# Kernel tuning notes

Hardware: AMD Instinct MI355X
Metric: run time of the kernel (lower is better)

Reference implementation:

```python
import jax, jax.numpy as jnp
import numpy as np

N = 240000
B = 2
GRID = (480, 360, 32)
NUM_CLASS = 20
IGNORE_LABEL = 0
MINB = np.array([0.0, -np.pi, -4.0], np.float32)
MAXB = np.array([50.0, np.pi, 2.0], np.float32)
EPS = 1e-5


def setup_inputs() -> dict:
    key = jax.random.key(0)
    ks = jax.random.split(key, 32)
    d = {}
    d['pt_fea'] = jax.random.normal(ks[0], (N, 6), jnp.float32)
    # cylindrical coords (rho, phi, z) uniformly inside the volume
    u = jax.random.uniform(ks[1], (N, 3), jnp.float32)
    d['xyz'] = u * jnp.asarray(MAXB - MINB) + jnp.asarray(MINB)
    d['batch_idx'] = jnp.sort(jax.random.randint(ks[2], (N,), 0, B)).astype(jnp.int64)
    d['pt_lab'] = jax.random.randint(ks[3], (N,), 0, NUM_CLASS).astype(jnp.int64)
    d['shuffled_ind'] = jnp.arange(N, dtype=jnp.int64)  # identity perm (deterministic)
    i = 4
    for name, c in [('bn0', 9), ('bn1', 64), ('bn2', 128), ('bn3', 256)]:
        d[name + '_g'] = jax.random.uniform(ks[i], (c,), jnp.float32, 0.5, 1.5); i += 1
        d[name + '_b'] = jax.random.normal(ks[i], (c,), jnp.float32) * 0.1; i += 1
        d[name + '_m'] = jax.random.normal(ks[i], (c,), jnp.float32) * 0.1; i += 1
        d[name + '_v'] = jax.random.uniform(ks[i], (c,), jnp.float32, 0.5, 1.5); i += 1
    for name, (fi, fo) in [('1', (9, 64)), ('2', (64, 128)), ('3', (128, 256)), ('4', (256, 256))]:
        d['w' + name] = jax.random.normal(ks[i], (fi, fo), jnp.float32) / np.sqrt(fi); i += 1
        d['b' + name] = jax.random.normal(ks[i], (fo,), jnp.float32) * 0.01; i += 1
    d['wc'] = jax.random.normal(ks[i], (256, 16), jnp.float32) / 16.0; i += 1
    d['bc'] = jax.random.normal(ks[i], (16,), jnp.float32) * 0.01
    return d


def _bn(x, g, b, m, v):
    return (x - m) * (g * jax.lax.rsqrt(v + EPS)) + b


def _ppmodel(feat, bn0_g, bn0_b, bn0_m, bn0_v, w1, b1, bn1_g, bn1_b, bn1_m, bn1_v,
             w2, b2, bn2_g, bn2_b, bn2_m, bn2_v, w3, b3, bn3_g, bn3_b, bn3_m, bn3_v, w4, b4):
    x = _bn(feat, bn0_g, bn0_b, bn0_m, bn0_v)
    x = jax.nn.relu(_bn(x @ w1 + b1, bn1_g, bn1_b, bn1_m, bn1_v))
    x = jax.nn.relu(_bn(x @ w2 + b2, bn2_g, bn2_b, bn2_m, bn2_v))
    x = jax.nn.relu(_bn(x @ w3 + b3, bn3_g, bn3_b, bn3_m, bn3_v))
    return x @ w4 + b4  # [N, 256]


def reference(pt_fea, xyz, batch_idx, pt_lab, shuffled_ind,
              bn0_g, bn0_b, bn0_m, bn0_v, w1, b1, bn1_g, bn1_b, bn1_m, bn1_v,
              w2, b2, bn2_g, bn2_b, bn2_m, bn2_v, w3, b3, bn3_g, bn3_b, bn3_m, bn3_v,
              w4, b4, wc, bc):
    minb = jnp.asarray(MINB)
    maxb = jnp.asarray(MAXB)
    grid = jnp.asarray(np.array(GRID, np.float32))
    intervals = (maxb - minb) / (grid - 1.0)

    clamped = jnp.clip(xyz, minb, maxb)
    ind = jnp.floor((clamped - minb) / intervals).astype(jnp.int32)  # [N,3]
    voxel_centers = (ind.astype(jnp.float32) + 0.5) * intervals + minb
    rel_xyz = xyz - voxel_centers
    feat = jnp.concatenate([rel_xyz, pt_fea], axis=1)  # [N,9]

    bi = batch_idx.astype(jnp.int32)
    counts = jnp.full((B,) + GRID + (NUM_CLASS,), IGNORE_LABEL, jnp.int32)
    counts = counts.at[bi, ind[:, 0], ind[:, 1], ind[:, 2], pt_lab].add(1)
    voxel_labels = jnp.argmax(counts, axis=-1).astype(jnp.int32)  # [B,480,360,32]

    feat = feat[shuffled_ind]

    flat = ((bi.astype(jnp.int64) * GRID[0] + ind[:, 0]) * GRID[1] + ind[:, 1]) * GRID[2] + ind[:, 2]
    unq, unq_inv = jnp.unique(flat, size=N, fill_value=-1, return_inverse=True)
    unq_inv = unq_inv.reshape(-1)

    processed = _ppmodel(feat, bn0_g, bn0_b, bn0_m, bn0_v, w1, b1, bn1_g, bn1_b, bn1_m, bn1_v,
                         w2, b2, bn2_g, bn2_b, bn2_m, bn2_v, w3, b3, bn3_g, bn3_b, bn3_m, bn3_v, w4, b4)
    pooled = jax.ops.segment_max(processed, unq_inv, num_segments=N)
    seg_cnt = jax.ops.segment_sum(jnp.ones((N,), jnp.float32), unq_inv, num_segments=N)
    pooled = jnp.where(seg_cnt[:, None] > 0, pooled, 0.0)  # zero out empty (padded) segments

    processed_pooled = jax.nn.relu(pooled @ wc + bc)  # fea_compression

    cat_pt_ind = jnp.concatenate([batch_idx[:, None], ind.astype(jnp.int64)], axis=1)
    return (unq, processed_pooled, voxel_labels, cat_pt_ind)
```

## Files before the change

kernel.cpp:

```cpp
#include <hip/hip_runtime.h>
#include <stdint.h>

#define N_PTS 240000
#define NV    11059200
#define NWORDS 172800
#define NB_PT 938
#define NB_WORD 675
#define NBLK_MLP 3750
#define PA 264

typedef __bf16 bf16x8 __attribute__((ext_vector_type(8)));
typedef short  short8 __attribute__((ext_vector_type(8)));
typedef float  f32x4  __attribute__((ext_vector_type(4)));

__device__ __forceinline__ unsigned short f2bf(float f) {
  unsigned u = __builtin_bit_cast(unsigned, f);
  return (unsigned short)((u + 0x7FFFu + ((u >> 16) & 1u)) >> 16);
}
__device__ __forceinline__ float bf2f(unsigned short h) {
  unsigned u = ((unsigned)h) << 16;
  return __builtin_bit_cast(float, u);
}

__global__ void prep_vox_kernel(
    const float* __restrict__ bng0, const float* __restrict__ bnb0, const float* __restrict__ bnm0, const float* __restrict__ bnv0,
    const float* __restrict__ bng1, const float* __restrict__ bnb1, const float* __restrict__ bnm1, const float* __restrict__ bnv1,
    const float* __restrict__ bng2, const float* __restrict__ bnb2, const float* __restrict__ bnm2, const float* __restrict__ bnv2,
    const float* __restrict__ bng3, const float* __restrict__ bnb3, const float* __restrict__ bnm3, const float* __restrict__ bnv3,
    const float* __restrict__ w1, const float* __restrict__ b1,
    const float* __restrict__ w2, const float* __restrict__ b2,
    const float* __restrict__ w3, const float* __restrict__ b3,
    const float* __restrict__ w4, const float* __restrict__ wc,
    float* __restrict__ s0, float* __restrict__ t0, float* __restrict__ w1e, float* __restrict__ be1,
    float* __restrict__ be2, float* __restrict__ be3,
    unsigned short* __restrict__ w2t, unsigned short* __restrict__ w3t, unsigned short* __restrict__ w4t,
    unsigned short* __restrict__ wct,
    const float* __restrict__ xyz, const int* __restrict__ bidx,
    unsigned* __restrict__ flatkeys, unsigned long long* __restrict__ bitmap,
    float* __restrict__ out_cat, float* __restrict__ out_unq)
{
  if (blockIdx.x < 256) {
    const int id = blockIdx.x * 256 + threadIdx.x;
    { int c = id >> 8, k = id & 255; w4t[c * 256 + k] = f2bf(w4[k * 256 + c]); }
    if (id < 32768) { int c = id >> 7, k = id & 127;
      float s = bng3[c] * rsqrtf(bnv3[c] + 1e-5f);
      w3t[c * 128 + k] = f2bf(w3[k * 256 + c] * s); }
    if (id < 8192) { int c = id >> 6, k = id & 63;
      float s = bng2[c] * rsqrtf(bnv2[c] + 1e-5f);
      w2t[c * 64 + k] = f2bf(w2[k * 128 + c] * s); }
    if (id < 4096) { int c = id >> 8, k = id & 255;
      wct[c * 256 + k] = f2bf(wc[k * 16 + c]); }
    if (id < 576) { int k = id / 64, c = id % 64;
      float s = bng1[c] * rsqrtf(bnv1[c] + 1e-5f);
      w1e[k * 64 + c] = w1[k * 64 + c] * s; }
    if (id < 64)  { float s = bng1[id] * rsqrtf(bnv1[id] + 1e-5f); be1[id] = (b1[id] - bnm1[id]) * s + bnb1[id]; }
    if (id < 128) { float s = bng2[id] * rsqrtf(bnv2[id] + 1e-5f); be2[id] = (b2[id] - bnm2[id]) * s + bnb2[id]; }
    if (id < 256) { float s = bng3[id] * rsqrtf(bnv3[id] + 1e-5f); be3[id] = (b3[id] - bnm3[id]) * s + bnb3[id]; }
    if (id < 9)   { float s = bng0[id] * rsqrtf(bnv0[id] + 1e-5f); s0[id] = s; t0[id] = bnb0[id] - bnm0[id] * s; }
    return;
  }
  const int j = (blockIdx.x - 256) * 256 + threadIdx.x;
  if (j >= N_PTS) return;
  out_unq[j] = -1.0f;
  const float PI_F = 3.14159265358979323846f;
  const float minb[3] = {0.0f, -PI_F, -4.0f};
  const float maxb[3] = {50.0f, PI_F, 2.0f};
  const float gm1[3]  = {479.0f, 359.0f, 31.0f};
  int ind[3];
  #pragma unroll
  for (int d = 0; d < 3; ++d) {
    float itv = (maxb[d] - minb[d]) / gm1[d];
    float x  = xyz[(size_t)j * 3 + d];
    float cl = fminf(fmaxf(x, minb[d]), maxb[d]);
    ind[d] = (int)floorf((cl - minb[d]) / itv);
  }
  const int bi = bidx[j];
  const unsigned flat = ((unsigned)(bi * 480 + ind[0]) * 360u + (unsigned)ind[1]) * 32u + (unsigned)ind[2];
  flatkeys[j] = flat;
  atomicOr(&bitmap[flat >> 6], 1ull << (flat & 63u));
  float* oc = out_cat + (size_t)j * 4;
  oc[0] = (float)bi; oc[1] = (float)ind[0]; oc[2] = (float)ind[1]; oc[3] = (float)ind[2];
}

__global__ void reduce_words(const unsigned long long* __restrict__ bm, unsigned* __restrict__ bsums) {
  __shared__ unsigned sh[256];
  const int w = blockIdx.x * 256 + threadIdx.x;
  sh[threadIdx.x] = (unsigned)__popcll(bm[w]);
  __syncthreads();
  for (int s = 128; s > 0; s >>= 1) { if (threadIdx.x < s) sh[threadIdx.x] += sh[threadIdx.x + s]; __syncthreads(); }
  if (threadIdx.x == 0) bsums[blockIdx.x] = sh[0];
}

__global__ void scan_small(unsigned* __restrict__ d, int n) {
  __shared__ unsigned sh[1024];
  const int t = threadIdx.x;
  unsigned own = (t < n) ? d[t] : 0u;
  sh[t] = own; __syncthreads();
  for (int off = 1; off < 1024; off <<= 1) {
    unsigned v = (t >= off) ? sh[t - off] : 0u;
    __syncthreads(); sh[t] += v; __syncthreads();
  }
  if (t < n) d[t] = sh[t] - own;
}

__global__ void scatter_unq(const unsigned long long* __restrict__ bm, const unsigned* __restrict__ bsums,
                            unsigned* __restrict__ wordpref, unsigned* __restrict__ unqvals,
                            float* __restrict__ out_unq) {
  __shared__ unsigned sh[256];
  const int t = threadIdx.x;
  const int w = blockIdx.x * 256 + t;
  unsigned long long word = bm[w];
  unsigned own = (unsigned)__popcll(word);
  sh[t] = own; __syncthreads();
  for (int off = 1; off < 256; off <<= 1) {
    unsigned v = (t >= off) ? sh[t - off] : 0u;
    __syncthreads(); sh[t] += v; __syncthreads();
  }
  unsigned r = bsums[blockIdx.x] + sh[t] - own;
  wordpref[w] = r;
  while (word) {
    int b = __builtin_ctzll(word);
    unsigned id = (unsigned)w * 64u + (unsigned)b;
    unqvals[r] = id;
    out_unq[r] = (float)id;
    ++r;
    word &= word - 1;
  }
}

__global__ void inv_kernel(const unsigned* __restrict__ flatkeys, const unsigned long long* __restrict__ bm,
                           const unsigned* __restrict__ wordpref, const int* __restrict__ ptlab,
                           unsigned* __restrict__ unq_inv, unsigned* __restrict__ cnt, unsigned* __restrict__ counts) {
  const int j = blockIdx.x * 256 + threadIdx.x;
  if (j >= N_PTS) return;
  const unsigned f = flatkeys[j];
  const unsigned w = f >> 6, b = f & 63u;
  const unsigned r = wordpref[w] + (unsigned)__popcll(bm[w] & ((1ull << b) - 1ull));
  unq_inv[j] = r;
  atomicAdd(&cnt[r], 1u);
  const unsigned lab = (unsigned)ptlab[j];
  atomicAdd(&counts[(size_t)r * 10 + (lab >> 1)], 1u << ((lab & 1u) * 16));
}

__global__ void reduce_cnt(const unsigned* __restrict__ cnt, unsigned* __restrict__ bsums) {
  __shared__ unsigned sh[256];
  const int j = blockIdx.x * 256 + threadIdx.x;
  sh[threadIdx.x] = (j < N_PTS) ? cnt[j] : 0u;
  __syncthreads();
  for (int s = 128; s > 0; s >>= 1) { if (threadIdx.x < s) sh[threadIdx.x] += sh[threadIdx.x + s]; __syncthreads(); }
  if (threadIdx.x == 0) bsums[blockIdx.x] = sh[0];
}
__global__ void scan_cnt(const unsigned* __restrict__ cnt, const unsigned* __restrict__ bsums,
                         unsigned* __restrict__ off, unsigned* __restrict__ cur) {
  __shared__ unsigned sh[256];
  const int t = threadIdx.x;
  const int j = blockIdx.x * 256 + t;
  unsigned own = (j < N_PTS) ? cnt[j] : 0u;
  sh[t] = own; __syncthreads();
  for (int o = 1; o < 256; o <<= 1) {
    unsigned v = (t >= o) ? sh[t - o] : 0u;
    __syncthreads(); sh[t] += v; __syncthreads();
  }
  if (j < N_PTS) { unsigned e = bsums[blockIdx.x] + sh[t] - own; off[j] = e; cur[j] = e; }
}

__global__ void plist_labels_kernel(const unsigned* __restrict__ unq_inv, unsigned* __restrict__ cur,
                                    unsigned* __restrict__ plist,
                                    const unsigned* __restrict__ cnt, const unsigned* __restrict__ counts,
                                    const unsigned* __restrict__ unqvals, const float* __restrict__ bc,
                                    float* __restrict__ out_lab, float* __restrict__ out_pooled) {
  const int j = blockIdx.x * 256 + threadIdx.x;
  if (j >= N_PTS) return;
  plist[atomicAdd(&cur[unq_inv[j]], 1u)] = (unsigned)j;
  const int u = j;
  if (cnt[u] == 0) {
    #pragma unroll
    for (int c = 0; c < 16; ++c) out_pooled[(size_t)u * 16 + c] = fmaxf(bc[c], 0.f);
    return;
  }
  const unsigned* c = counts + (size_t)u * 10;
  int best = 0; unsigned bv = c[0] & 0xFFFFu;
  #pragma unroll
  for (int l = 1; l < 20; ++l) {
    unsigned v = (c[l >> 1] >> ((l & 1) * 16)) & 0xFFFFu;
    if (v > bv) { bv = v; best = l; }
  }
  out_lab[unqvals[u]] = (float)best;
}

template<int K, int C, bool RELU, bool MIDB>
__device__ __forceinline__ void gemm_stage(
    const unsigned short* __restrict__ Wt,
    const float* __restrict__ bias,
    const unsigned short* in,
    unsigned short* outp,
    int wave, int l15, int quad)
{
  constexpr int KC = K / 32;
  constexpr int NT = C / 64;
  f32x4 acc[4][NT];
  #pragma unroll
  for (int mt = 0; mt < 4; ++mt)
    #pragma unroll
    for (int nt = 0; nt < NT; ++nt) acc[mt][nt] = (f32x4){0.f, 0.f, 0.f, 0.f};
  const unsigned short* wp[NT];
  #pragma unroll
  for (int nt = 0; nt < NT; ++nt)
    wp[nt] = Wt + (size_t)(wave * 16 * NT + nt * 16 + l15) * K + quad * 8;
  #pragma unroll
  for (int kc = 0; kc < KC; ++kc) {
    bf16x8 b[NT];
    #pragma unroll
    for (int nt = 0; nt < NT; ++nt)
      b[nt] = __builtin_bit_cast(bf16x8, *(const short8*)(wp[nt] + kc * 32));
    #pragma unroll
    for (int mt = 0; mt < 4; ++mt) {
      bf16x8 a = __builtin_bit_cast(bf16x8, *(const short8*)&in[(mt * 16 + l15) * PA + kc * 32 + quad * 8]);
      #pragma unroll
      for (int nt = 0; nt < NT; ++nt)
        acc[mt][nt] = __builtin_amdgcn_mfma_f32_16x16x32_bf16(b[nt], a, acc[mt][nt], 0, 0, 0);
    }
  }
  if (MIDB) __syncthreads();
  #pragma unroll
  for (int mt = 0; mt < 4; ++mt)
    #pragma unroll
    for (int nt = 0; nt < NT; ++nt) {
      const int cbase = wave * 16 * NT + nt * 16 + quad * 4;
      const f32x4 bs = *(const f32x4*)&bias[cbase];
      unsigned short h[4];
      #pragma unroll
      for (int r = 0; r < 4; ++r) {
        float y = acc[mt][nt][r] + bs[r];
        if (RELU) y = fmaxf(y, 0.f);
        h[r] = f2bf(y);
      }
      uint2 pk; pk.x = (unsigned)h[0] | ((unsigned)h[1] << 16);
      pk.y = (unsigned)h[2] | ((unsigned)h[3] << 16);
      *(uint2*)&outp[(mt * 16 + l15) * PA + cbase] = pk;
    }
  __syncthreads();
}

__global__ __launch_bounds__(256, 4) void mlp_pool_kernel(
    const float* __restrict__ ptfea, const float* __restrict__ xyz, const int* __restrict__ shuf,
    const unsigned* __restrict__ plist, const unsigned* __restrict__ unq_inv,
    const unsigned* __restrict__ offv, const unsigned* __restrict__ cnt,
    const float* __restrict__ s0, const float* __restrict__ t0,
    const float* __restrict__ w1e, const float* __restrict__ be1,
    const unsigned short* __restrict__ w2t, const float* __restrict__ be2,
    const unsigned short* __restrict__ w3t, const float* __restrict__ be3,
    const unsigned short* __restrict__ w4t, const float* __restrict__ b4,
    const unsigned short* __restrict__ wct, const float* __restrict__ bc,
    unsigned short* __restrict__ partials, float* __restrict__ out_pooled)
{
  __shared__ __align__(16) unsigned short buf[64 * PA];
  __shared__ int segs[64];
  __shared__ int jrows[64];
  __shared__ int s_alast;
  __shared__ int s_nrun;
  __shared__ unsigned short s_runs[32];
  __shared__ unsigned char s_lead[64], s_comp[64];
  const int tid  = threadIdx.x;
  const int wave = tid >> 6, lane = tid & 63;
  const int l15 = lane & 15, quad = lane >> 4;
  const int row0 = blockIdx.x * 64;

  if (tid == 0) { s_alast = 0; s_nrun = 0; }
  if (lane < 16) {
    const int r = wave * 16 + lane;
    int j = (int)plist[row0 + r];
    jrows[r] = j;
    segs[r] = (int)unq_inv[j];
  }

  {
    const int r = wave * 16 + (lane >> 2), part = lane & 3;
    const int sj = shuf[jrows[r]];
    const float PI_F = 3.14159265358979323846f;
    const float minb[3] = {0.0f, -PI_F, -4.0f};
    const float maxb[3] = {50.0f, PI_F, 2.0f};
    const float gm1[3]  = {479.0f, 359.0f, 31.0f};
    float x0[9];
    #pragma unroll
    for (int d = 0; d < 3; ++d) {
      float itv = (maxb[d] - minb[d]) / gm1[d];
      float x   = xyz[(size_t)sj * 3 + d];
      float cl  = fminf(fmaxf(x, minb[d]), maxb[d]);
      float fi  = floorf((cl - minb[d]) / itv);
      float center = (fi + 0.5f) * itv + minb[d];
      x0[d] = (x - center) * s0[d] + t0[d];
    }
    #pragma unroll
    for (int d = 0; d < 6; ++d) x0[3 + d] = ptfea[(size_t)sj * 6 + d] * s0[3 + d] + t0[3 + d];
    unsigned short h[16];
    #pragma unroll
    for (int ci = 0; ci < 16; ++ci) {
      float acc = be1[part * 16 + ci];
      #pragma unroll
      for (int k = 0; k < 9; ++k) acc += x0[k] * w1e[k * 64 + part * 16 + ci];
      h[ci] = f2bf(fmaxf(acc, 0.0f));
    }
    *(short8*)&buf[r * PA + part * 16]     = *(short8*)&h[0];
    *(short8*)&buf[r * PA + part * 16 + 8] = *(short8*)&h[8];
  }
  __syncthreads();

  gemm_stage< 64, 128, true,  false>(w2t, be2, buf,       buf + 136, wave, l15, quad);
  gemm_stage<128, 256, true,  true >(w3t, be3, buf + 136, buf,       wave, l15, quad);
  gemm_stage<256, 256, false, true >(w4t, b4,  buf,       buf,       wave, l15, quad);

  if (tid < 64) {
    const int r = tid;
    bool lead = (r == 0) || (segs[r] != segs[r - 1]);
    s_lead[r] = lead ? 1 : 0;
    unsigned char comp = 0;
    int e = r + 1;
    if (lead) {
      atomicMax(&s_alast, r);
      while (e < 64 && segs[e] == segs[r]) ++e;
      const unsigned s = (unsigned)segs[r];
      comp = (offv[s] == (unsigned)(row0 + r) && offv[s] + cnt[s] == (unsigned)(row0 + e)) ? 1 : 0;
    }
    s_comp[r] = comp;
    const bool multi = lead && (e - r) > 1;
    unsigned long long mm = __ballot(multi);
    if (multi) {
      int idx = (int)__popcll(mm & ((1ull << r) - 1ull));
      s_runs[idx] = (unsigned short)((r << 8) | e);
    }
    if (tid == 0) s_nrun = (int)__popcll(mm);
  }
  __syncthreads();

  {
    const int n = s_nrun;
    for (int i = 0; i < n; ++i) {
      const int re = s_runs[i];
      const int r = re >> 8, e = re & 255;
      float m = bf2f(buf[r * PA + tid]);
      for (int rr = r + 1; rr < e; ++rr) m = fmaxf(m, bf2f(buf[rr * PA + tid]));
      buf[r * PA + tid] = f2bf(m);
    }
  }
  __syncthreads();

  {
    const int c = tid;
    const int alast = s_alast;
    const size_t b2 = (size_t)blockIdx.x * 2;
    if (!s_comp[0])     partials[b2 * 256 + c]       = buf[0 * PA + c];
    if (!s_comp[alast]) partials[(b2 + 1) * 256 + c] = buf[alast * PA + c];
  }

  {
    const unsigned short* wp = wct + l15 * 256 + quad * 8;
    f32x4 acc = (f32x4){0.f, 0.f, 0.f, 0.f};
    #pragma unroll
    for (int kc = 0; kc < 256; kc += 32) {
      bf16x8 w = __builtin_bit_cast(bf16x8, *(const short8*)(wp + kc));
      bf16x8 x = __builtin_bit_cast(bf16x8, *(const short8*)&buf[(wave * 16 + l15) * PA + kc + quad * 8]);
      acc = __builtin_amdgcn_mfma_f32_16x16x32_bf16(w, x, acc, 0, 0, 0);
    }
    const int r1 = wave * 16 + l15;
    if (s_lead[r1] && s_comp[r1]) {
      const f32x4 bcv = *(const f32x4*)&bc[quad * 4];
      f32x4 v;
      #pragma unroll
      for (int r = 0; r < 4; ++r) v[r] = fmaxf(acc[r] + bcv[r], 0.f);
      *(f32x4*)&out_pooled[(size_t)segs[r1] * 16 + quad * 4] = v;
    }
  }
}

__global__ __launch_bounds__(256) void merge_kernel(
    const unsigned* __restrict__ plist, const unsigned* __restrict__ unq_inv,
    const unsigned* __restrict__ offv, const unsigned* __restrict__ cnt,
    const unsigned short* __restrict__ partials,
    const float* __restrict__ wc, const float* __restrict__ bc,
    float* __restrict__ out_pooled)
{
  __shared__ float pooled[256];
  __shared__ float psum[256];
  const int b = blockIdx.x;
  const unsigned s = unq_inv[plist[(size_t)b * 64 + 63]];
  const unsigned o = offv[s], e = o + cnt[s];
  if ((o >> 6) != (unsigned)b) return;
  if (e <= (unsigned)(b + 1) * 64) return;
  const int B1 = (int)((e - 1) >> 6);
  const int c = threadIdx.x;
  float m = bf2f(partials[((size_t)2 * b + 1) * 256 + c]);
  for (int bb = b + 1; bb <= B1; ++bb)
    m = fmaxf(m, bf2f(partials[(size_t)2 * bb * 256 + c]));
  pooled[c] = m;
  __syncthreads();
  const int co = c & 15, kg = c >> 4;
  float p = 0.f;
  #pragma unroll
  for (int k = kg * 16; k < kg * 16 + 16; ++k) p += pooled[k] * wc[k * 16 + co];
  psum[c] = p;
  __syncthreads();
  if (c < 16) {
    float acc = bc[c];
    #pragma unroll
    for (int g = 0; g < 16; ++g) acc += psum[g * 16 + c];
    out_pooled[(size_t)s * 16 + c] = fmaxf(acc, 0.f);
  }
}

extern "C" void kernel_launch(void* const* d_in, const int* in_sizes, int n_in,
                              void* d_out, int out_size, void* d_ws, size_t ws_size,
                              hipStream_t stream)
{
  const float* pt_fea = (const float*)d_in[0];
  const float* xyz    = (const float*)d_in[1];
  const int*   bidx   = (const int*)d_in[2];
  const int*   ptlab  = (const int*)d_in[3];
  const int*   shuf   = (const int*)d_in[4];
  const float* bng0 = (const float*)d_in[5],  *bnb0 = (const float*)d_in[6],  *bnm0 = (const float*)d_in[7],  *bnv0 = (const float*)d_in[8];
  const float* bng1 = (const float*)d_in[9],  *bnb1 = (const float*)d_in[10], *bnm1 = (const float*)d_in[11], *bnv1 = (const float*)d_in[12];
  const float* bng2 = (const float*)d_in[13], *bnb2 = (const float*)d_in[14], *bnm2 = (const float*)d_in[15], *bnv2 = (const float*)d_in[16];
  const float* bng3 = (const float*)d_in[17], *bnb3 = (const float*)d_in[18], *bnm3 = (const float*)d_in[19], *bnv3 = (const float*)d_in[20];
  const float* w1 = (const float*)d_in[21], *b1 = (const float*)d_in[22];
  const float* w2 = (const float*)d_in[23], *b2 = (const float*)d_in[24];
  const float* w3 = (const float*)d_in[25], *b3 = (const float*)d_in[26];
  const float* w4 = (const float*)d_in[27], *b4 = (const float*)d_in[28];
  const float* wc = (const float*)d_in[29], *bc = (const float*)d_in[30];

  float* out        = (float*)d_out;
  float* out_unq    = out;
  float* out_pooled = out + 240000;
  float* out_lab    = out + 4080000;
  float* out_cat    = out + 15139200;

  char* wsb = (char*)d_ws;
  size_t o = 0;
  auto alloc = [&](size_t bytes) -> void* { void* p = wsb + o; o = (o + bytes + 255) & ~(size_t)255; return p; };
  unsigned long long* bitmap = (unsigned long long*)alloc((size_t)NWORDS * 8);
  unsigned* cnt    = (unsigned*)alloc((size_t)N_PTS * 4);
  unsigned* counts = (unsigned*)alloc((size_t)N_PTS * 10 * 4);
  const size_t zero_bytes = o;
  float* s0  = (float*)alloc(9 * 4);
  float* t0  = (float*)alloc(9 * 4);
  float* w1e = (float*)alloc(576 * 4);
  float* be1 = (float*)alloc(64 * 4);
  float* be2 = (float*)alloc(128 * 4);
  float* be3 = (float*)alloc(256 * 4);
  unsigned short* w2t = (unsigned short*)alloc(8192 * 2);
  unsigned short* w3t = (unsigned short*)alloc(32768 * 2);
  unsigned short* w4t = (unsigned short*)alloc(65536 * 2);
  unsigned short* wct = (unsigned short*)alloc(4096 * 2);
  unsigned* flatkeys = (unsigned*)alloc((size_t)N_PTS * 4);
  unsigned* unq_inv  = (unsigned*)alloc((size_t)N_PTS * 4);
  unsigned* unqvals  = (unsigned*)alloc((size_t)N_PTS * 4);
  unsigned* offv     = (unsigned*)alloc((size_t)N_PTS * 4);
  unsigned* cur      = (unsigned*)alloc((size_t)N_PTS * 4);
  unsigned* plist    = (unsigned*)alloc((size_t)N_PTS * 4);
  unsigned* wordpref = (unsigned*)alloc((size_t)NWORDS * 4);
  unsigned* bsumA    = (unsigned*)alloc(NB_WORD * 4);
  unsigned* bsumB    = (unsigned*)alloc(NB_PT * 4);
  unsigned short* partials = (unsigned short*)alloc((size_t)NBLK_MLP * 2 * 256 * 2);

  hipMemsetAsync(bitmap, 0, zero_bytes, stream);
  hipMemsetAsync(out_lab, 0, (size_t)NV * 4, stream);

  prep_vox_kernel<<<256 + NB_PT, 256, 0, stream>>>(
      bng0, bnb0, bnm0, bnv0, bng1, bnb1, bnm1, bnv1,
      bng2, bnb2, bnm2, bnv2, bng3, bnb3, bnm3, bnv3,
      w1, b1, w2, b2, w3, b3, w4, wc,
      s0, t0, w1e, be1, be2, be3, w2t, w3t, w4t, wct,
      xyz, bidx, flatkeys, bitmap, out_cat, out_unq);
  reduce_words<<<NB_WORD, 256, 0, stream>>>(bitmap, bsumA);
  scan_small<<<1, 1024, 0, stream>>>(bsumA, NB_WORD);
  scatter_unq<<<NB_WORD, 256, 0, stream>>>(bitmap, bsumA, wordpref, unqvals, out_unq);
  inv_kernel<<<NB_PT, 256, 0, stream>>>(flatkeys, bitmap, wordpref, ptlab, unq_inv, cnt, counts);
  reduce_cnt<<<NB_PT, 256, 0, stream>>>(cnt, bsumB);
  scan_small<<<1, 1024, 0, stream>>>(bsumB, NB_PT);
  scan_cnt<<<NB_PT, 256, 0, stream>>>(cnt, bsumB, offv, cur);
  plist_labels_kernel<<<NB_PT, 256, 0, stream>>>(unq_inv, cur, plist, cnt, counts, unqvals, bc,
                                                 out_lab, out_pooled);
  mlp_pool_kernel<<<NBLK_MLP, 256, 0, stream>>>(pt_fea, xyz, shuf, plist, unq_inv, offv, cnt,
                                                s0, t0, w1e, be1, w2t, be2, w3t, be3, w4t, b4,
                                                wct, bc, partials, out_pooled);
  merge_kernel<<<NBLK_MLP, 256, 0, stream>>>(plist, unq_inv, offv, cnt, partials, wc, bc, out_pooled);
}
```

Measured before the change: 369.5 us.

## Fuse block-sum scans and move voxel label voting into pooling kernels

```diff
diff --git a/kernel.cpp b/kernel.cpp
--- a/kernel.cpp
+++ b/kernel.cpp
@@ -20,6 +20,16 @@
 __device__ __forceinline__ float bf2f(unsigned short h) {
   unsigned u = ((unsigned)h) << 16;
   return __builtin_bit_cast(float, u);
+}
+
+__device__ __forceinline__ unsigned block_sum(unsigned v, unsigned* s4, int t) {
+  #pragma unroll
+  for (int o = 32; o; o >>= 1) v += __shfl_down(v, o);
+  if ((t & 63) == 0) s4[t >> 6] = v;
+  __syncthreads();
+  unsigned r = s4[0] + s4[1] + s4[2] + s4[3];
+  __syncthreads();
+  return r;
 }
 
 __global__ void prep_vox_kernel(
@@ -91,24 +101,14 @@
   if (threadIdx.x == 0) bsums[blockIdx.x] = sh[0];
 }
 
-__global__ void scan_small(unsigned* __restrict__ d, int n) {
-  __shared__ unsigned sh[1024];
-  const int t = threadIdx.x;
-  unsigned own = (t < n) ? d[t] : 0u;
-  sh[t] = own; __syncthreads();
-  for (int off = 1; off < 1024; off <<= 1) {
-    unsigned v = (t >= off) ? sh[t - off] : 0u;
-    __syncthreads(); sh[t] += v; __syncthreads();
-  }
-  if (t < n) d[t] = sh[t] - own;
-}
-
-__global__ void scatter_unq(const unsigned long long* __restrict__ bm, const unsigned* __restrict__ bsums,
-                            unsigned* __restrict__ wordpref, unsigned* __restrict__ unqvals,
-                            float* __restrict__ out_unq) {
+__global__ __launch_bounds__(256) void scatter_unq(
+    const unsigned long long* __restrict__ bm, const unsigned* __restrict__ bsums,
+    unsigned* __restrict__ wordpref, unsigned* __restrict__ unqvals, float* __restrict__ out_unq)
+{
   __shared__ unsigned sh[256];
-  const int t = threadIdx.x;
-  const int w = blockIdx.x * 256 + t;
+  __shared__ unsigned s4[4];
+  const int t = threadIdx.x, b = blockIdx.x;
+  const int w = b * 256 + t;
   unsigned long long word = bm[w];
   unsigned own = (unsigned)__popcll(word);
   sh[t] = own; __syncthreads();
@@ -116,11 +116,14 @@
     unsigned v = (t >= off) ? sh[t - off] : 0u;
     __syncthreads(); sh[t] += v; __syncthreads();
   }
-  unsigned r = bsums[blockIdx.x] + sh[t] - own;
+  unsigned v = 0;
+  for (int i = t; i < b; i += 256) v += bsums[i];
+  const unsigned excl = block_sum(v, s4, t);
+  unsigned r = excl + sh[t] - own;
   wordpref[w] = r;
   while (word) {
-    int b = __builtin_ctzll(word);
-    unsigned id = (unsigned)w * 64u + (unsigned)b;
+    int bit = __builtin_ctzll(word);
+    unsigned id = (unsigned)w * 64u + (unsigned)bit;
     unqvals[r] = id;
     out_unq[r] = (float)id;
     ++r;
@@ -129,8 +132,8 @@
 }
 
 __global__ void inv_kernel(const unsigned* __restrict__ flatkeys, const unsigned long long* __restrict__ bm,
-                           const unsigned* __restrict__ wordpref, const int* __restrict__ ptlab,
-                           unsigned* __restrict__ unq_inv, unsigned* __restrict__ cnt, unsigned* __restrict__ counts) {
+                           const unsigned* __restrict__ wordpref,
+                           unsigned* __restrict__ unq_inv, unsigned* __restrict__ cnt) {
   const int j = blockIdx.x * 256 + threadIdx.x;
   if (j >= N_PTS) return;
   const unsigned f = flatkeys[j];
@@ -138,8 +141,6 @@
   const unsigned r = wordpref[w] + (unsigned)__popcll(bm[w] & ((1ull << b) - 1ull));
   unq_inv[j] = r;
   atomicAdd(&cnt[r], 1u);
-  const unsigned lab = (unsigned)ptlab[j];
-  atomicAdd(&counts[(size_t)r * 10 + (lab >> 1)], 1u << ((lab & 1u) * 16));
 }
 
 __global__ void reduce_cnt(const unsigned* __restrict__ cnt, unsigned* __restrict__ bsums) {
@@ -150,42 +151,38 @@
   for (int s = 128; s > 0; s >>= 1) { if (threadIdx.x < s) sh[threadIdx.x] += sh[threadIdx.x + s]; __syncthreads(); }
   if (threadIdx.x == 0) bsums[blockIdx.x] = sh[0];
 }
-__global__ void scan_cnt(const unsigned* __restrict__ cnt, const unsigned* __restrict__ bsums,
-                         unsigned* __restrict__ off, unsigned* __restrict__ cur) {
+
+__global__ __launch_bounds__(256) void scan_cnt(
+    const unsigned* __restrict__ cnt, const unsigned* __restrict__ bsums,
+    unsigned* __restrict__ off, unsigned* __restrict__ cur)
+{
   __shared__ unsigned sh[256];
-  const int t = threadIdx.x;
-  const int j = blockIdx.x * 256 + t;
+  __shared__ unsigned s4[4];
+  const int t = threadIdx.x, b = blockIdx.x;
+  const int j = b * 256 + t;
   unsigned own = (j < N_PTS) ? cnt[j] : 0u;
   sh[t] = own; __syncthreads();
   for (int o = 1; o < 256; o <<= 1) {
     unsigned v = (t >= o) ? sh[t - o] : 0u;
     __syncthreads(); sh[t] += v; __syncthreads();
   }
-  if (j < N_PTS) { unsigned e = bsums[blockIdx.x] + sh[t] - own; off[j] = e; cur[j] = e; }
-}
-
-__global__ void plist_labels_kernel(const unsigned* __restrict__ unq_inv, unsigned* __restrict__ cur,
-                                    unsigned* __restrict__ plist,
-                                    const unsigned* __restrict__ cnt, const unsigned* __restrict__ counts,
-                                    const unsigned* __restrict__ unqvals, const float* __restrict__ bc,
-                                    float* __restrict__ out_lab, float* __restrict__ out_pooled) {
+  unsigned v = 0;
+  for (int i = t; i < b; i += 256) v += bsums[i];
+  const unsigned excl = block_sum(v, s4, t);
+  if (j < N_PTS) { unsigned e = excl + sh[t] - own; off[j] = e; cur[j] = e; }
+}
+
+__global__ void plist_fill_kernel(const unsigned* __restrict__ unq_inv, unsigned* __restrict__ cur,
+                                  unsigned* __restrict__ plist,
+                                  const unsigned* __restrict__ cnt, const float* __restrict__ bc,
+                                  float* __restrict__ out_pooled) {
   const int j = blockIdx.x * 256 + threadIdx.x;
   if (j >= N_PTS) return;
   plist[atomicAdd(&cur[unq_inv[j]], 1u)] = (unsigned)j;
-  const int u = j;
-  if (cnt[u] == 0) {
-    #pragma unroll
-    for (int c = 0; c < 16; ++c) out_pooled[(size_t)u * 16 + c] = fmaxf(bc[c], 0.f);
-    return;
-  }
-  const unsigned* c = counts + (size_t)u * 10;
-  int best = 0; unsigned bv = c[0] & 0xFFFFu;
-  #pragma unroll
-  for (int l = 1; l < 20; ++l) {
-    unsigned v = (c[l >> 1] >> ((l & 1) * 16)) & 0xFFFFu;
-    if (v > bv) { bv = v; best = l; }
-  }
-  out_lab[unqvals[u]] = (float)best;
+  if (cnt[j] == 0) {
+    #pragma unroll
+    for (int c = 0; c < 16; ++c) out_pooled[(size_t)j * 16 + c] = fmaxf(bc[c], 0.f);
+  }
 }
 
 template<int K, int C, bool RELU, bool MIDB>
@@ -246,13 +243,15 @@
     const float* __restrict__ ptfea, const float* __restrict__ xyz, const int* __restrict__ shuf,
     const unsigned* __restrict__ plist, const unsigned* __restrict__ unq_inv,
     const unsigned* __restrict__ offv, const unsigned* __restrict__ cnt,
+    const int* __restrict__ ptlab, const unsigned* __restrict__ unqvals,
     const float* __restrict__ s0, const float* __restrict__ t0,
     const float* __restrict__ w1e, const float* __restrict__ be1,
     const unsigned short* __restrict__ w2t, const float* __restrict__ be2,
     const unsigned short* __restrict__ w3t, const float* __restrict__ be3,
     const unsigned short* __restrict__ w4t, const float* __restrict__ b4,
     const unsigned short* __restrict__ wct, const float* __restrict__ bc,
-    unsigned short* __restrict__ partials, float* __restrict__ out_pooled)
+    unsigned short* __restrict__ partials, float* __restrict__ out_pooled,
+    float* __restrict__ out_lab)
 {
   __shared__ __align__(16) unsigned short buf[64 * PA];
   __shared__ int segs[64];
@@ -323,6 +322,20 @@
       comp = (offv[s] == (unsigned)(row0 + r) && offv[s] + cnt[s] == (unsigned)(row0 + e)) ? 1 : 0;
     }
     s_comp[r] = comp;
+    if (comp) {
+      int bestl;
+      if (e - r == 1) bestl = ptlab[jrows[r]];
+      else {
+        int bestc = 0; bestl = 32;
+        for (int i = r; i < e; ++i) {
+          const int li = ptlab[jrows[i]];
+          int cc = 0;
+          for (int k2 = r; k2 < e; ++k2) cc += (ptlab[jrows[k2]] == li) ? 1 : 0;
+          if (cc > bestc || (cc == bestc && li < bestl)) { bestc = cc; bestl = li; }
+        }
+      }
+      out_lab[unqvals[segs[r]]] = (float)bestl;
+    }
     const bool multi = lead && (e - r) > 1;
     unsigned long long mm = __ballot(multi);
     if (multi) {
@@ -377,8 +390,9 @@
     const unsigned* __restrict__ plist, const unsigned* __restrict__ unq_inv,
     const unsigned* __restrict__ offv, const unsigned* __restrict__ cnt,
     const unsigned short* __restrict__ partials,
+    const int* __restrict__ ptlab, const unsigned* __restrict__ unqvals,
     const float* __restrict__ wc, const float* __restrict__ bc,
-    float* __restrict__ out_pooled)
+    float* __restrict__ out_pooled, float* __restrict__ out_lab)
 {
   __shared__ float pooled[256];
   __shared__ float psum[256];
@@ -405,6 +419,16 @@
     #pragma unroll
     for (int g = 0; g < 16; ++g) acc += psum[g * 16 + c];
     out_pooled[(size_t)s * 16 + c] = fmaxf(acc, 0.f);
+  }
+  if (c == 0) {
+    int bestc = 0, bestl = 32;
+    for (unsigned i = o; i < e; ++i) {
+      const int li = ptlab[plist[i]];
+      int cc = 0;
+      for (unsigned k2 = o; k2 < e; ++k2) cc += (ptlab[plist[k2]] == li) ? 1 : 0;
+      if (cc > bestc || (cc == bestc && li < bestl)) { bestc = cc; bestl = li; }
+    }
+    out_lab[unqvals[s]] = (float)bestl;
   }
 }
 
@@ -438,7 +462,6 @@
   auto alloc = [&](size_t bytes) -> void* { void* p = wsb + o; o = (o + bytes + 255) & ~(size_t)255; return p; };
   unsigned long long* bitmap = (unsigned long long*)alloc((size_t)NWORDS * 8);
   unsigned* cnt    = (unsigned*)alloc((size_t)N_PTS * 4);
-  unsigned* counts = (unsigned*)alloc((size_t)N_PTS * 10 * 4);
   const size_t zero_bytes = o;
   float* s0  = (float*)alloc(9 * 4);
   float* t0  = (float*)alloc(9 * 4);
@@ -471,16 +494,15 @@
       s0, t0, w1e, be1, be2, be3, w2t, w3t, w4t, wct,
       xyz, bidx, flatkeys, bitmap, out_cat, out_unq);
   reduce_words<<<NB_WORD, 256, 0, stream>>>(bitmap, bsumA);
-  scan_small<<<1, 1024, 0, stream>>>(bsumA, NB_WORD);
   scatter_unq<<<NB_WORD, 256, 0, stream>>>(bitmap, bsumA, wordpref, unqvals, out_unq);
-  inv_kernel<<<NB_PT, 256, 0, stream>>>(flatkeys, bitmap, wordpref, ptlab, unq_inv, cnt, counts);
+  inv_kernel<<<NB_PT, 256, 0, stream>>>(flatkeys, bitmap, wordpref, unq_inv, cnt);
   reduce_cnt<<<NB_PT, 256, 0, stream>>>(cnt, bsumB);
-  scan_small<<<1, 1024, 0, stream>>>(bsumB, NB_PT);
   scan_cnt<<<NB_PT, 256, 0, stream>>>(cnt, bsumB, offv, cur);
-  plist_labels_kernel<<<NB_PT, 256, 0, stream>>>(unq_inv, cur, plist, cnt, counts, unqvals, bc,
-                                                 out_lab, out_pooled);
+  plist_fill_kernel<<<NB_PT, 256, 0, stream>>>(unq_inv, cur, plist, cnt, bc, out_pooled);
   mlp_pool_kernel<<<NBLK_MLP, 256, 0, stream>>>(pt_fea, xyz, shuf, plist, unq_inv, offv, cnt,
+                                                ptlab, unqvals,
                                                 s0, t0, w1e, be1, w2t, be2, w3t, be3, w4t, b4,
-                                                wct, bc, partials, out_pooled);
-  merge_kernel<<<NBLK_MLP, 256, 0, stream>>>(plist, unq_inv, offv, cnt, partials, wc, bc, out_pooled);
-}
+                                                wct, bc, partials, out_pooled, out_lab);
+  merge_kernel<<<NBLK_MLP, 256, 0, stream>>>(plist, unq_inv, offv, cnt, partials,
+                                             ptlab, unqvals, wc, bc, out_pooled, out_lab);
+}
```

New measurement: 352.0 us. -4.7%, faster.
